# Kernel optimization log

Hardware: AMD Instinct MI355X
Metric: run time of the kernel (lower is better)

Reference implementation:

```python
import jax, jax.numpy as jnp
import numpy as np

NUM_Q_HEADS = 64
NUM_KV_HEADS = 8
HEAD_DIM = 64
HIDDEN = 2880
SLIDING_WINDOW = 128
ROPE_WAVELENGTH = 10000.0
NEG_INF = jnp.float32(-1e9)


def _rope(x, start_index=0):
    # x: (b, s, n, h). yarn with scaling_factor=1.0 == standard RoPE (split-half rotate).
    s, h = x.shape[1], x.shape[-1]
    inv_freq = 1.0 / (ROPE_WAVELENGTH ** (jnp.arange(0, h, 2, dtype=jnp.float32) / h))
    pos = jnp.arange(s, dtype=jnp.float32) + start_index
    freqs = pos[:, None] * inv_freq[None, :]  # (s, h/2)
    cos = jnp.concatenate([jnp.cos(freqs), jnp.cos(freqs)], axis=-1)[None, :, None, :]
    sin = jnp.concatenate([jnp.sin(freqs), jnp.sin(freqs)], axis=-1)[None, :, None, :]
    x1, x2 = jnp.split(x, 2, axis=-1)
    rot = jnp.concatenate([-x2, x1], axis=-1)
    return x * cos + rot * sin


def setup_inputs() -> dict:
    key = jax.random.key(0)
    ks = jax.random.split(key, 9)
    b, s = 1, 2048
    scale = 0.02
    hidden_states = jax.random.normal(ks[0], (b, s, HIDDEN), jnp.float32)
    Wq = jax.random.normal(ks[1], (HIDDEN, NUM_Q_HEADS, HEAD_DIM), jnp.float32) * scale
    Wk = jax.random.normal(ks[2], (HIDDEN, NUM_KV_HEADS, HEAD_DIM), jnp.float32) * scale
    Wv = jax.random.normal(ks[3], (HIDDEN, NUM_KV_HEADS, HEAD_DIM), jnp.float32) * scale
    Wo = jax.random.normal(ks[4], (NUM_Q_HEADS, HEAD_DIM, HIDDEN), jnp.float32) * scale
    bq = jnp.zeros((NUM_Q_HEADS, HEAD_DIM), jnp.float32)
    bk = jnp.zeros((NUM_KV_HEADS, HEAD_DIM), jnp.float32)
    bv = jnp.zeros((NUM_KV_HEADS, HEAD_DIM), jnp.float32)
    bo = jnp.zeros((HIDDEN,), jnp.float32)
    sinks = jax.random.normal(ks[5], (NUM_Q_HEADS,), jnp.float32) * 0.05
    attention_mask = jnp.tril(jnp.ones((s, s), bool))[None]  # causal, (b, q, k)
    return dict(hidden_states=hidden_states, Wq=Wq, bq=bq, Wk=Wk, bk=bk, Wv=Wv,
                bv=bv, Wo=Wo, bo=bo, sinks=sinks, attention_mask=attention_mask)


def reference(hidden_states, Wq, bq, Wk, bk, Wv, bv, Wo, bo, sinks, attention_mask):
    b, s, _ = hidden_states.shape
    inv_norm = 1.0 / np.sqrt(HEAD_DIM).astype(np.float32)
    # QKV projections (EinsumDense with bias)
    q = jnp.einsum('bqm,muh->bquh', hidden_states, Wq) + bq
    k = jnp.einsum('bkm,mvh->bkvh', hidden_states, Wk) + bk
    v = jnp.einsum('bkm,mvh->bkvh', hidden_states, Wv) + bv
    # rotary_dim == head_dim (even), so RoPE applies to the full head dim
    q = _rope(q)
    k = _rope(k)
    # GQA: repeat kv heads
    groups = NUM_Q_HEADS // NUM_KV_HEADS
    k = jnp.repeat(k, groups, axis=2)
    v = jnp.repeat(v, groups, axis=2)
    scores = jnp.einsum('bquh,bkuh->buqk', q, k) * inv_norm
    # sliding-window mask: keep kv_pos >= q_pos - window
    qpos = jnp.arange(s)
    swin = qpos[None, :] >= qpos[:, None] - SLIDING_WINDOW  # (q, k)
    scores = jnp.where(swin[None, None], scores, NEG_INF)
    scores = jnp.where(attention_mask[:, None], scores, NEG_INF)
    # sink-token logit per head appended as extra kv column
    sink = jnp.broadcast_to(sinks.reshape(1, NUM_Q_HEADS, 1, 1), (b, NUM_Q_HEADS, s, 1))
    logits = jnp.concatenate([scores, sink], axis=-1)
    m = jax.lax.stop_gradient(jnp.max(logits, axis=-1, keepdims=True))
    probs = jax.nn.softmax(logits - m, axis=-1)[..., :-1]  # drop sink column
    attn = jnp.einsum('buqk,bkuh->bquh', probs, v)
    return jnp.einsum('bquh,uhm->bqm', attn, Wo) + bo
```

## Files before the change

kernel.cpp:

```cpp
#include <hip/hip_runtime.h>
#include <cstdint>

typedef __attribute__((ext_vector_type(4))) float f32x4;
typedef __attribute__((ext_vector_type(8))) short bf16x8;

#define HIDDEN 2880
#define SEQ 2048
#define QKV_N 5120
#define WIN 128

__device__ __forceinline__ ushort f2bf(float f) {
  uint32_t u = __builtin_bit_cast(uint32_t, f);
  u += 0x7fff + ((u >> 16) & 1);
  return (ushort)(u >> 16);
}
__device__ __forceinline__ float bf2f(ushort h) {
  uint32_t u = ((uint32_t)h) << 16;
  return __builtin_bit_cast(float, u);
}

__global__ void conv_kernel(const float* __restrict__ in, ushort* __restrict__ out, int n) {
  int i = (blockIdx.x * blockDim.x + threadIdx.x) * 8;
  if (i >= n) return;
  float4 a = *(const float4*)(in + i);
  float4 b = *(const float4*)(in + i + 4);
  bf16x8 o;
  o[0] = (short)f2bf(a.x); o[1] = (short)f2bf(a.y); o[2] = (short)f2bf(a.z); o[3] = (short)f2bf(a.w);
  o[4] = (short)f2bf(b.x); o[5] = (short)f2bf(b.y); o[6] = (short)f2bf(b.z); o[7] = (short)f2bf(b.w);
  *(bf16x8*)(out + i) = o;
}

__global__ __launch_bounds__(256) void tconv2_kernel(const float* __restrict__ in, ushort* __restrict__ out,
                                                     int C, int out_ld, int out_row_off) {
  __shared__ ushort tile[64][68];
  int c0 = blockIdx.x * 64, r0 = blockIdx.y * 64;
  int t = threadIdx.x;
  int lr = t >> 4;
  int lc = (t & 15) * 4;
#pragma unroll
  for (int i = 0; i < 4; ++i) {
    float4 v = *(const float4*)&in[(size_t)(r0 + i * 16 + lr) * C + c0 + lc];
    ushort4 o;
    o.x = f2bf(v.x); o.y = f2bf(v.y); o.z = f2bf(v.z); o.w = f2bf(v.w);
    *(ushort4*)&tile[i * 16 + lr][lc] = o;
  }
  __syncthreads();
  int rr0 = (t & 7) * 8;
#pragma unroll
  for (int i2 = 0; i2 < 2; ++i2) {
    int cc = i2 * 32 + (t >> 3);
    bf16x8 o;
#pragma unroll
    for (int j = 0; j < 8; ++j) o[j] = (short)tile[rr0 + j][cc];
    *(bf16x8*)&out[(size_t)(out_row_off + c0 + cc) * out_ld + r0 + rr0] = o;
  }
}

__global__ void biascat_kernel(const float* __restrict__ bq, const float* __restrict__ bk,
                               const float* __restrict__ bv, float* __restrict__ out) {
  int i = blockIdx.x * blockDim.x + threadIdx.x;
  if (i >= QKV_N) return;
  float v = (i < 4096) ? bq[i] : (i < 4608) ? bk[i - 4096] : bv[i - 4608];
  out[i] = v;
}

__global__ void ropetab_kernel(float2* __restrict__ tab) {
  int i = blockIdx.x * blockDim.x + threadIdx.x;
  int s = i >> 5, d = i & 31;
  float inv = powf(10000.0f, -(float)d / 32.0f);
  float f = (float)s * inv;
  tab[i] = make_float2(cosf(f), sinf(f));
}

__global__ __launch_bounds__(256) void vt_kernel(const ushort* __restrict__ qkv, ushort* __restrict__ vt) {
  __shared__ ushort tile[64][80];
  int kv0 = blockIdx.x * 64, d0 = blockIdx.y * 64;
  int t = threadIdx.x;
#pragma unroll
  for (int p = 0; p < 2; ++p) {
    int lr = p * 32 + (t >> 3);
    *(bf16x8*)&tile[lr][(t & 7) * 8] =
        *(const bf16x8*)&qkv[(size_t)(kv0 + lr) * QKV_N + 4608 + d0 + (t & 7) * 8];
  }
  __syncthreads();
#pragma unroll
  for (int p = 0; p < 2; ++p) {
    int dl = p * 32 + (t >> 3);
    bf16x8 o;
#pragma unroll
    for (int jj = 0; jj < 8; ++jj) o[jj] = (short)tile[(t & 7) * 8 + jj][dl];
    *(bf16x8*)&vt[(size_t)(d0 + dl) * 2048 + kv0 + (t & 7) * 8] = o;
  }
}

template <int BN, bool OUT_BF16>
__global__ __launch_bounds__(256, 2) void gemm4w_kernel(
    const ushort* __restrict__ A, const ushort* __restrict__ Bt,
    const float* __restrict__ bias, void* __restrict__ Cv,
    int K, int lda, int ldb, int ldc) {
  constexpr int NFRAG = BN / 32;
  constexpr int BHALF = BN * 64;
  constexpr int BCHUNKS = BHALF / 1024;
  constexpr int BUFBYTES = 16384 + 2 * BHALF;
  __shared__ __align__(16) char ldsbuf[2 * BUFBYTES];

  const int cpx = gridDim.x >> 3;
  const int wg = ((int)blockIdx.x & 7) * cpx + ((int)blockIdx.x >> 3);
  const int mtile = wg & 15, ntile = wg >> 4;
  const int m0 = mtile * 128, n0 = ntile * BN;

  const int tid = threadIdx.x, wv = tid >> 6, l = tid & 63;
  const int wm = wv >> 1, wn = wv & 1;
  const int r = l & 15, g = l >> 4;

  const int c = l ^ ((l >> 3) & 3);
  const ushort* gA0 = A + (size_t)(m0 + (c >> 2)) * lda + (c & 3) * 8;
  const ushort* gB0 = Bt + (size_t)(n0 + (c >> 2)) * ldb + (c & 3) * 8;

  const int gsw = (g * 16) ^ (((r >> 1) & 3) << 4);
  const int aOff = (wm * 64 + r) * 64 + gsw;
  const int bOff = (wn * (NFRAG * 16) + r) * 64 + gsw;

  auto sA = [&](int nb, int kg, int kh) {
#pragma unroll
    for (int j = 0; j < 2; ++j) {
      int cid = j * 4 + wv;
      __builtin_amdgcn_global_load_lds(
          (const __attribute__((address_space(1))) void*)(const void*)(gA0 + (size_t)cid * 16 * lda + kg),
          (__attribute__((address_space(3))) void*)&ldsbuf[nb * BUFBYTES + kh * 8192 + cid * 1024], 16, 0, 0);
    }
  };
  auto sB = [&](int nb, int kg, int kh) {
#pragma unroll
    for (int j = 0; j < (BCHUNKS + 3) / 4; ++j) {
      int cid = j * 4 + wv;
      if (cid < BCHUNKS)
        __builtin_amdgcn_global_load_lds(
            (const __attribute__((address_space(1))) void*)(const void*)(gB0 + (size_t)cid * 16 * ldb + kg),
            (__attribute__((address_space(3))) void*)&ldsbuf[nb * BUFBYTES + 16384 + kh * BHALF + cid * 1024],
            16, 0, 0);
    }
  };

#define BAR() __builtin_amdgcn_s_barrier()
#define LGKMC(N)                                                       \
  do {                                                                 \
    asm volatile("s_waitcnt lgkmcnt(%0)" ::"n"(N) : "memory");         \
    __builtin_amdgcn_sched_barrier(0);                                 \
  } while (0)
#define WAITV0() asm volatile("s_waitcnt vmcnt(0)" ::: "memory")

  f32x4 acc[4][NFRAG] = {};
  const int nt = K >> 6;

  sA(0, 0, 0); sA(0, 32, 1); sB(0, 0, 0); sB(0, 32, 1);
  WAITV0();
  BAR();

  for (int t = 0; t < nt; ++t) {
    const int bufOff = (t & 1) * BUFBYTES;
    const int nb = (t & 1) ^ 1;
    bf16x8 aq0[4], bq0[NFRAG], aq1[4], bq1[NFRAG];
#pragma unroll
    for (int nf = 0; nf < NFRAG; ++nf)
      bq0[nf] = *(const bf16x8*)&ldsbuf[bufOff + 16384 + bOff + nf * 1024];
#pragma unroll
    for (int mi = 0; mi < 4; ++mi)
      aq0[mi] = *(const bf16x8*)&ldsbuf[bufOff + aOff + mi * 1024];
    __builtin_amdgcn_sched_barrier(0);
#pragma unroll
    for (int nf = 0; nf < NFRAG; ++nf)
      bq1[nf] = *(const bf16x8*)&ldsbuf[bufOff + 16384 + BHALF + bOff + nf * 1024];
#pragma unroll
    for (int mi = 0; mi < 4; ++mi)
      aq1[mi] = *(const bf16x8*)&ldsbuf[bufOff + 8192 + aOff + mi * 1024];
    if (t + 1 < nt) {
      const int kn = (t + 1) * 64;
      sA(nb, kn, 0); sA(nb, kn + 32, 1);
      sB(nb, kn, 0); sB(nb, kn + 32, 1);
    }
    LGKMC(4 + NFRAG);
    __builtin_amdgcn_s_setprio(1);
#pragma unroll
    for (int mi = 0; mi < 4; ++mi)
#pragma unroll
      for (int nf = 0; nf < NFRAG; ++nf)
        acc[mi][nf] = __builtin_amdgcn_mfma_f32_16x16x32_bf16(aq0[mi], bq0[nf], acc[mi][nf], 0, 0, 0);
    __builtin_amdgcn_s_setprio(0);
    LGKMC(0);
    __builtin_amdgcn_s_setprio(1);
#pragma unroll
    for (int mi = 0; mi < 4; ++mi)
#pragma unroll
      for (int nf = 0; nf < NFRAG; ++nf)
        acc[mi][nf] = __builtin_amdgcn_mfma_f32_16x16x32_bf16(aq1[mi], bq1[nf], acc[mi][nf], 0, 0, 0);
    __builtin_amdgcn_s_setprio(0);
    WAITV0();
    BAR();
  }

#pragma unroll
  for (int mf2 = 0; mf2 < 4; ++mf2) {
#pragma unroll
    for (int nf = 0; nf < NFRAG; ++nf) {
      int cc = n0 + wn * (NFRAG * 16) + nf * 16 + r;
      float b = bias[cc];
#pragma unroll
      for (int j = 0; j < 4; ++j) {
        int rrow = m0 + wm * 64 + mf2 * 16 + g * 4 + j;
        float v = acc[mf2][nf][j] + b;
        if (OUT_BF16) ((ushort*)Cv)[(size_t)rrow * ldc + cc] = f2bf(v);
        else ((float*)Cv)[(size_t)rrow * ldc + cc] = v;
      }
    }
  }
#undef BAR
#undef LGKMC
#undef WAITV0
}

__global__ __launch_bounds__(512, 4) void attn_kernel(
    const ushort* __restrict__ qkv, const ushort* __restrict__ vt,
    const float* __restrict__ sinks, const float2* __restrict__ tab,
    ushort* __restrict__ out) {
  __shared__ __align__(16) char lds[54272];
  const int kh = blockIdx.y;
  const int q0 = blockIdx.x * 32;
  const int kvw0 = q0 - 128;
  const int tid = threadIdx.x, w = tid >> 6, l = tid & 63;
  const int r = l & 15, g = l >> 4;
  const int h = kh * 8 + w;

  if (tid < 256) ((uint32_t*)(lds + 40960))[tid] = 0;

#pragma unroll
  for (int it = 0; it < 4; ++it) {
    int c = it * 512 + tid;
    if (c < 640) {
      int row = c >> 2, ch = c & 3;
      int kv = kvw0 + row;
      bf16x8 v1 = {}, v2 = {};
      if (kv >= 0) {
        const ushort* kb = &qkv[(size_t)kv * QKV_N + 4096 + kh * 64 + ch * 8];
        bf16x8 x1 = *(const bf16x8*)kb;
        bf16x8 x2 = *(const bf16x8*)(kb + 32);
#pragma unroll
        for (int i = 0; i < 8; ++i) {
          float2 cs = tab[(kv << 5) + ch * 8 + i];
          float a = bf2f((ushort)x1[i]), b = bf2f((ushort)x2[i]);
          v1[i] = (short)f2bf(a * cs.x - b * cs.y);
          v2[i] = (short)f2bf(b * cs.x + a * cs.y);
        }
      }
      int b1 = (row * 128 + ch * 16) ^ ((row & 7) << 4);
      int b2 = (row * 128 + (ch + 4) * 16) ^ ((row & 7) << 4);
      *(bf16x8*)(lds + b1) = v1;
      *(bf16x8*)(lds + b2) = v2;
    } else if (c < 1920) {
      int cv = c - 640;
      int row = cv / 20, ch = cv - (cv / 20) * 20;
      int kv = kvw0 + ch * 8;
      bf16x8 vv = {};
      if (kv >= 0) vv = *(const bf16x8*)&vt[(size_t)(kh * 64 + row) * 2048 + kv];
      int byte = (row * 320 + ch * 16) ^ ((row & 7) << 4);
      *(bf16x8*)(lds + 20480 + byte) = vv;
    }
  }
  __syncthreads();

  char* Pw = lds + 41984 + w * 1536;
  const float snk = sinks[h];

#pragma unroll
  for (int si = 0; si < 2; ++si) {
    const ushort* qb = &qkv[(size_t)(q0 + si * 16 + r) * QKV_N + h * 64 + g * 8];
    bf16x8 qf0 = *(const bf16x8*)qb;
    bf16x8 qf1 = *(const bf16x8*)(qb + 32);
    {
      int s = q0 + si * 16 + r;
      bf16x8 t0, t1;
#pragma unroll
      for (int i = 0; i < 8; ++i) {
        float2 cs = tab[(s << 5) + g * 8 + i];
        float a = bf2f((ushort)qf0[i]), b = bf2f((ushort)qf1[i]);
        t0[i] = (short)f2bf(a * cs.x - b * cs.y);
        t1[i] = (short)f2bf(b * cs.x + a * cs.y);
      }
      qf0 = t0; qf1 = t1;
    }

    f32x4 S[9];
    float mx[4] = {-3e30f, -3e30f, -3e30f, -3e30f};
#pragma unroll
    for (int tt = 0; tt < 9; ++tt) {
      int kvloc = (si + tt) * 16 + r;
      int b0 = (kvloc * 128 + g * 16) ^ ((kvloc & 7) << 4);
      int b1 = (kvloc * 128 + 64 + g * 16) ^ ((kvloc & 7) << 4);
      bf16x8 kf0 = *(const bf16x8*)(lds + b0);
      bf16x8 kf1 = *(const bf16x8*)(lds + b1);
      f32x4 s = {};
      s = __builtin_amdgcn_mfma_f32_16x16x32_bf16(qf0, kf0, s, 0, 0, 0);
      s = __builtin_amdgcn_mfma_f32_16x16x32_bf16(qf1, kf1, s, 0, 0, 0);
      int kvc = kvw0 + kvloc;
#pragma unroll
      for (int j = 0; j < 4; ++j) {
        int qr = q0 + si * 16 + g * 4 + j;
        bool valid = (kvc >= 0) && (kvc <= qr) && (kvc >= qr - WIN);
        float v = valid ? s[j] * 0.125f : -1e30f;
        s[j] = v;
        mx[j] = fmaxf(mx[j], v);
      }
      S[tt] = s;
    }
#pragma unroll
    for (int off = 1; off < 16; off <<= 1)
#pragma unroll
      for (int j = 0; j < 4; ++j) mx[j] = fmaxf(mx[j], __shfl_xor(mx[j], off, 64));
    float m[4], sum[4] = {0, 0, 0, 0};
#pragma unroll
    for (int j = 0; j < 4; ++j) m[j] = fmaxf(mx[j], snk);
#pragma unroll
    for (int tt = 0; tt < 9; ++tt)
#pragma unroll
      for (int j = 0; j < 4; ++j) {
        float p = (S[tt][j] > -1e29f) ? __expf(S[tt][j] - m[j]) : 0.0f;
        S[tt][j] = p;
        sum[j] += p;
      }
#pragma unroll
    for (int off = 1; off < 16; off <<= 1)
#pragma unroll
      for (int j = 0; j < 4; ++j) sum[j] += __shfl_xor(sum[j], off, 64);
    float rinv[4];
#pragma unroll
    for (int j = 0; j < 4; ++j) rinv[j] = 1.0f / (sum[j] + __expf(snk - m[j]));

    f32x4 acc[4] = {};
#pragma unroll
    for (int ks = 0; ks < 5; ++ks) {
#pragma unroll
      for (int c2 = 0; c2 < 2; ++c2) {
        int tt = 2 * ks + c2;
#pragma unroll
        for (int j = 0; j < 4; ++j) {
          float pv = (tt <= 8) ? S[tt][j] * rinv[j] : 0.0f;
          *(ushort*)(Pw + ((g * 4 + j) * 48 + c2 * 16 + r) * 2) = f2bf(pv);
        }
      }
      bf16x8 pa = *(const bf16x8*)(Pw + (r * 48 + g * 8) * 2);
#pragma unroll
      for (int ni = 0; ni < 4; ++ni) {
        int row = ni * 16 + r;
        int byte = (row * 320 + (si * 16 + ks * 32 + g * 8) * 2) ^ ((row & 7) << 4);
        bf16x8 vb = *(const bf16x8*)(lds + 20480 + byte);
        acc[ni] = __builtin_amdgcn_mfma_f32_16x16x32_bf16(pa, vb, acc[ni], 0, 0, 0);
      }
    }
#pragma unroll
    for (int ni = 0; ni < 4; ++ni)
#pragma unroll
      for (int j = 0; j < 4; ++j)
        out[(size_t)(q0 + si * 16 + g * 4 + j) * 4096 + h * 64 + ni * 16 + r] = f2bf(acc[ni][j]);
  }
}

extern "C" void kernel_launch(void* const* d_in, const int* in_sizes, int n_in,
                              void* d_out, int out_size, void* d_ws, size_t ws_size,
                              hipStream_t stream) {
  const float* hs = (const float*)d_in[0];
  const float* Wq = (const float*)d_in[1];
  const float* bq = (const float*)d_in[2];
  const float* Wk = (const float*)d_in[3];
  const float* bk = (const float*)d_in[4];
  const float* Wv = (const float*)d_in[5];
  const float* bv = (const float*)d_in[6];
  const float* Wo = (const float*)d_in[7];
  const float* bo = (const float*)d_in[8];
  const float* sinks = (const float*)d_in[9];
  float* out = (float*)d_out;

  char* ws = (char*)d_ws;
  ushort* hs_bf   = (ushort*)(ws + 0);
  ushort* vt_g    = (ushort*)(ws + 0);
  ushort* wqkv_t  = (ushort*)(ws + 11796480);
  ushort* attn    = (ushort*)(ws + 11796480);
  ushort* wo_t    = (ushort*)(ws + 41287680);
  ushort* qkv     = (ushort*)(ws + 66453504);
  float*  bias_all= (float*)(ws + 87425024);
  float2* tab     = (float2*)(ws + 87445504);

  conv_kernel<<<5898240 / 8 / 256, 256, 0, stream>>>(hs, hs_bf, 5898240);
  tconv2_kernel<<<dim3(64, 45), 256, 0, stream>>>(Wq, wqkv_t, 4096, 2880, 0);
  tconv2_kernel<<<dim3(8, 45), 256, 0, stream>>>(Wk, wqkv_t, 512, 2880, 4096);
  tconv2_kernel<<<dim3(8, 45), 256, 0, stream>>>(Wv, wqkv_t, 512, 2880, 4608);
  tconv2_kernel<<<dim3(45, 64), 256, 0, stream>>>(Wo, wo_t, 2880, 4096, 0);
  biascat_kernel<<<20, 256, 0, stream>>>(bq, bk, bv, bias_all);
  ropetab_kernel<<<2048 * 32 / 256, 256, 0, stream>>>(tab);

  gemm4w_kernel<160, true><<<512, 256, 0, stream>>>(hs_bf, wqkv_t, bias_all, qkv,
                                                    2880, 2880, 2880, 5120);
  vt_kernel<<<dim3(32, 8), 256, 0, stream>>>(qkv, vt_g);
  attn_kernel<<<dim3(64, 8), 512, 0, stream>>>(qkv, vt_g, sinks, tab, attn);
  gemm4w_kernel<192, false><<<240, 256, 0, stream>>>(attn, wo_t, bo, out,
                                                     4096, 4096, 4096, 2880);
}
```

Baseline: 202.7 us.

## Fuse prep kernels into one launch, simplify GEMM LDS loads, retile output GEMM

Merges the seven preprocessing launches (hidden-state conversion, four weight transposes, bias concat, RoPE table) into a single block-indexed prep kernel to cut launch overhead. The GEMM main loop now issues global prefetch first, then loads and consumes each K-half in turn with a full lgkmcnt(0) wait, instead of preloading both halves and overlapping the second half's LDS reads with the first half's MFMAs. The output projection GEMM changes from BN=192 with 240 blocks to BN=160 with 288 blocks. Exposing the LDS latency for each K-half could slow the GEMMs, and the prep kernel's branchy dispatch mixes uneven block workloads.

```diff
diff --git a/kernel.cpp b/kernel.cpp
--- a/kernel.cpp
+++ b/kernel.cpp
@@ -19,22 +19,10 @@
   return __builtin_bit_cast(float, u);
 }
 
-__global__ void conv_kernel(const float* __restrict__ in, ushort* __restrict__ out, int n) {
-  int i = (blockIdx.x * blockDim.x + threadIdx.x) * 8;
-  if (i >= n) return;
-  float4 a = *(const float4*)(in + i);
-  float4 b = *(const float4*)(in + i + 4);
-  bf16x8 o;
-  o[0] = (short)f2bf(a.x); o[1] = (short)f2bf(a.y); o[2] = (short)f2bf(a.z); o[3] = (short)f2bf(a.w);
-  o[4] = (short)f2bf(b.x); o[5] = (short)f2bf(b.y); o[6] = (short)f2bf(b.z); o[7] = (short)f2bf(b.w);
-  *(bf16x8*)(out + i) = o;
-}
-
-__global__ __launch_bounds__(256) void tconv2_kernel(const float* __restrict__ in, ushort* __restrict__ out,
-                                                     int C, int out_ld, int out_row_off) {
-  __shared__ ushort tile[64][68];
-  int c0 = blockIdx.x * 64, r0 = blockIdx.y * 64;
-  int t = threadIdx.x;
+__device__ __forceinline__ void tconv_tile(const float* __restrict__ in, ushort* __restrict__ out,
+                                           int C, int out_ld, int out_row_off,
+                                           int bx, int by, int t, ushort (*tile)[68]) {
+  int c0 = bx * 64, r0 = by * 64;
   int lr = t >> 4;
   int lc = (t & 15) * 4;
 #pragma unroll
@@ -56,20 +44,47 @@
   }
 }
 
-__global__ void biascat_kernel(const float* __restrict__ bq, const float* __restrict__ bk,
-                               const float* __restrict__ bv, float* __restrict__ out) {
-  int i = blockIdx.x * blockDim.x + threadIdx.x;
-  if (i >= QKV_N) return;
-  float v = (i < 4096) ? bq[i] : (i < 4608) ? bk[i - 4096] : bv[i - 4608];
-  out[i] = v;
-}
-
-__global__ void ropetab_kernel(float2* __restrict__ tab) {
-  int i = blockIdx.x * blockDim.x + threadIdx.x;
-  int s = i >> 5, d = i & 31;
-  float inv = powf(10000.0f, -(float)d / 32.0f);
-  float f = (float)s * inv;
-  tab[i] = make_float2(cosf(f), sinf(f));
+__global__ __launch_bounds__(256) void prep_kernel(
+    const float* __restrict__ hs, const float* __restrict__ Wq, const float* __restrict__ Wk,
+    const float* __restrict__ Wv, const float* __restrict__ Wo,
+    const float* __restrict__ bq, const float* __restrict__ bk, const float* __restrict__ bv,
+    ushort* __restrict__ hs_bf, ushort* __restrict__ wqkv_t, ushort* __restrict__ wo_t,
+    float* __restrict__ bias_all, float2* __restrict__ tab) {
+  __shared__ ushort tile[64][68];
+  const int b = blockIdx.x, t = threadIdx.x;
+  if (b < 2880) {
+    int i = (b * 256 + t) * 8;
+    float4 a = *(const float4*)(hs + i);
+    float4 c = *(const float4*)(hs + i + 4);
+    bf16x8 o;
+    o[0] = (short)f2bf(a.x); o[1] = (short)f2bf(a.y); o[2] = (short)f2bf(a.z); o[3] = (short)f2bf(a.w);
+    o[4] = (short)f2bf(c.x); o[5] = (short)f2bf(c.y); o[6] = (short)f2bf(c.z); o[7] = (short)f2bf(c.w);
+    *(bf16x8*)(hs_bf + i) = o;
+  } else if (b < 5760) {
+    int idx = b - 2880;
+    tconv_tile(Wq, wqkv_t, 4096, 2880, 0, idx & 63, idx >> 6, t, tile);
+  } else if (b < 6120) {
+    int idx = b - 5760;
+    tconv_tile(Wk, wqkv_t, 512, 2880, 4096, idx & 7, idx >> 3, t, tile);
+  } else if (b < 6480) {
+    int idx = b - 6120;
+    tconv_tile(Wv, wqkv_t, 512, 2880, 4608, idx & 7, idx >> 3, t, tile);
+  } else if (b < 9360) {
+    int idx = b - 6480;
+    tconv_tile(Wo, wo_t, 2880, 4096, 0, idx % 45, idx / 45, t, tile);
+  } else if (b < 9380) {
+    int i = (b - 9360) * 256 + t;
+    if (i < QKV_N) {
+      float v = (i < 4096) ? bq[i] : (i < 4608) ? bk[i - 4096] : bv[i - 4608];
+      bias_all[i] = v;
+    }
+  } else {
+    int i = (b - 9380) * 256 + t;
+    int s = i >> 5, d = i & 31;
+    float inv = powf(10000.0f, -(float)d / 32.0f);
+    float f = (float)s * inv;
+    tab[i] = make_float2(cosf(f), sinf(f));
+  }
 }
 
 __global__ __launch_bounds__(256) void vt_kernel(const ushort* __restrict__ qkv, ushort* __restrict__ vt) {
@@ -92,6 +107,14 @@
     *(bf16x8*)&vt[(size_t)(d0 + dl) * 2048 + kv0 + (t & 7) * 8] = o;
   }
 }
+
+#define LGKM0()                                              \
+  do {                                                       \
+    asm volatile("s_waitcnt lgkmcnt(0)" ::: "memory");       \
+    __builtin_amdgcn_sched_barrier(0);                       \
+  } while (0)
+#define WAITV0() asm volatile("s_waitcnt vmcnt(0)" ::: "memory")
+#define BAR() __builtin_amdgcn_s_barrier()
 
 template <int BN, bool OUT_BF16>
 __global__ __launch_bounds__(256, 2) void gemm4w_kernel(
@@ -142,14 +165,6 @@
     }
   };
 
-#define BAR() __builtin_amdgcn_s_barrier()
-#define LGKMC(N)                                                       \
-  do {                                                                 \
-    asm volatile("s_waitcnt lgkmcnt(%0)" ::"n"(N) : "memory");         \
-    __builtin_amdgcn_sched_barrier(0);                                 \
-  } while (0)
-#define WAITV0() asm volatile("s_waitcnt vmcnt(0)" ::: "memory")
-
   f32x4 acc[4][NFRAG] = {};
   const int nt = K >> 6;
 
@@ -160,41 +175,29 @@
   for (int t = 0; t < nt; ++t) {
     const int bufOff = (t & 1) * BUFBYTES;
     const int nb = (t & 1) ^ 1;
-    bf16x8 aq0[4], bq0[NFRAG], aq1[4], bq1[NFRAG];
-#pragma unroll
-    for (int nf = 0; nf < NFRAG; ++nf)
-      bq0[nf] = *(const bf16x8*)&ldsbuf[bufOff + 16384 + bOff + nf * 1024];
-#pragma unroll
-    for (int mi = 0; mi < 4; ++mi)
-      aq0[mi] = *(const bf16x8*)&ldsbuf[bufOff + aOff + mi * 1024];
-    __builtin_amdgcn_sched_barrier(0);
-#pragma unroll
-    for (int nf = 0; nf < NFRAG; ++nf)
-      bq1[nf] = *(const bf16x8*)&ldsbuf[bufOff + 16384 + BHALF + bOff + nf * 1024];
-#pragma unroll
-    for (int mi = 0; mi < 4; ++mi)
-      aq1[mi] = *(const bf16x8*)&ldsbuf[bufOff + 8192 + aOff + mi * 1024];
     if (t + 1 < nt) {
       const int kn = (t + 1) * 64;
       sA(nb, kn, 0); sA(nb, kn + 32, 1);
       sB(nb, kn, 0); sB(nb, kn + 32, 1);
     }
-    LGKMC(4 + NFRAG);
-    __builtin_amdgcn_s_setprio(1);
-#pragma unroll
-    for (int mi = 0; mi < 4; ++mi)
+#pragma unroll
+    for (int kh = 0; kh < 2; ++kh) {
+      bf16x8 aq[4], bq[NFRAG];
 #pragma unroll
       for (int nf = 0; nf < NFRAG; ++nf)
-        acc[mi][nf] = __builtin_amdgcn_mfma_f32_16x16x32_bf16(aq0[mi], bq0[nf], acc[mi][nf], 0, 0, 0);
-    __builtin_amdgcn_s_setprio(0);
-    LGKMC(0);
-    __builtin_amdgcn_s_setprio(1);
-#pragma unroll
-    for (int mi = 0; mi < 4; ++mi)
-#pragma unroll
-      for (int nf = 0; nf < NFRAG; ++nf)
-        acc[mi][nf] = __builtin_amdgcn_mfma_f32_16x16x32_bf16(aq1[mi], bq1[nf], acc[mi][nf], 0, 0, 0);
-    __builtin_amdgcn_s_setprio(0);
+        bq[nf] = *(const bf16x8*)&ldsbuf[bufOff + 16384 + kh * BHALF + bOff + nf * 1024];
+#pragma unroll
+      for (int mi = 0; mi < 4; ++mi)
+        aq[mi] = *(const bf16x8*)&ldsbuf[bufOff + kh * 8192 + aOff + mi * 1024];
+      LGKM0();
+      __builtin_amdgcn_s_setprio(1);
+#pragma unroll
+      for (int mi = 0; mi < 4; ++mi)
+#pragma unroll
+        for (int nf = 0; nf < NFRAG; ++nf)
+          acc[mi][nf] = __builtin_amdgcn_mfma_f32_16x16x32_bf16(aq[mi], bq[nf], acc[mi][nf], 0, 0, 0);
+      __builtin_amdgcn_s_setprio(0);
+    }
     WAITV0();
     BAR();
   }
@@ -214,9 +217,6 @@
       }
     }
   }
-#undef BAR
-#undef LGKMC
-#undef WAITV0
 }
 
 __global__ __launch_bounds__(512, 4) void attn_kernel(
@@ -389,18 +389,13 @@
   float*  bias_all= (float*)(ws + 87425024);
   float2* tab     = (float2*)(ws + 87445504);
 
-  conv_kernel<<<5898240 / 8 / 256, 256, 0, stream>>>(hs, hs_bf, 5898240);
-  tconv2_kernel<<<dim3(64, 45), 256, 0, stream>>>(Wq, wqkv_t, 4096, 2880, 0);
-  tconv2_kernel<<<dim3(8, 45), 256, 0, stream>>>(Wk, wqkv_t, 512, 2880, 4096);
-  tconv2_kernel<<<dim3(8, 45), 256, 0, stream>>>(Wv, wqkv_t, 512, 2880, 4608);
-  tconv2_kernel<<<dim3(45, 64), 256, 0, stream>>>(Wo, wo_t, 2880, 4096, 0);
-  biascat_kernel<<<20, 256, 0, stream>>>(bq, bk, bv, bias_all);
-  ropetab_kernel<<<2048 * 32 / 256, 256, 0, stream>>>(tab);
+  prep_kernel<<<9636, 256, 0, stream>>>(hs, Wq, Wk, Wv, Wo, bq, bk, bv,
+                                        hs_bf, wqkv_t, wo_t, bias_all, tab);
 
   gemm4w_kernel<160, true><<<512, 256, 0, stream>>>(hs_bf, wqkv_t, bias_all, qkv,
                                                     2880, 2880, 2880, 5120);
   vt_kernel<<<dim3(32, 8), 256, 0, stream>>>(qkv, vt_g);
   attn_kernel<<<dim3(64, 8), 512, 0, stream>>>(qkv, vt_g, sinks, tab, attn);
-  gemm4w_kernel<192, false><<<240, 256, 0, stream>>>(attn, wo_t, bo, out,
+  gemm4w_kernel<160, false><<<288, 256, 0, stream>>>(attn, wo_t, bo, out,
                                                      4096, 4096, 4096, 2880);
 }
```

Measured after the change: 192.1 us (median of 2 runs). 5.2% less time.
